# Optimization experiments

Measured on AMD Instinct MI355X. Metric: run time of the kernel, lower is better.

## Reference

```python
import jax, jax.numpy as jnp
import numpy as np

N, E, F_IN, H, MH, C, G = 100000, 3200000, 128, 32, 64, 10, 64

def _seg_sum(data, ids, num):
    return jax.ops.segment_sum(data, ids, num_segments=num)

def gcn_conv(x, row, col, ew, W, b, n):
    # PyG GCNConv: linear first, then self-loops + symmetric edge-weight norm + scatter-add
    h = x @ W  # [N, H]
    loop = jnp.arange(n)
    r = jnp.concatenate([row, loop])
    c = jnp.concatenate([col, loop])
    w = jnp.concatenate([ew, jnp.ones((n,), dtype=ew.dtype)])
    deg = _seg_sum(w, c, n)
    dinv = jnp.where(deg > 0, jax.lax.rsqrt(deg), 0.0)
    norm = dinv[r] * w * dinv[c]  # [E+N]
    out = _seg_sum(norm[:, None] * h[r], c, n)  # scatter to targets
    return out + b

def setup_inputs():
    key = jax.random.key(0)
    ks = jax.random.split(key, 16)
    inp = {
        "x": jax.random.normal(ks[0], (N, F_IN), dtype=jnp.float32),
        "edge_index": jax.random.randint(ks[1], (2, E), 0, N, dtype=jnp.int64),
        "edge_weight": jax.random.uniform(ks[2], (E,), dtype=jnp.float32),
        "batch": jnp.sort(jax.random.randint(ks[3], (N,), 0, G, dtype=jnp.int64)),
    }
    def lin(k, i, o):
        s = 1.0 / np.sqrt(i)
        k1, k2 = jax.random.split(k)
        return (jax.random.uniform(k1, (i, o), minval=-s, maxval=s, dtype=jnp.float32),
                jax.random.uniform(k2, (o,), minval=-s, maxval=s, dtype=jnp.float32))
    inp["W1"], inp["b1"] = lin(ks[4], F_IN, H)
    inp["W2"], inp["b2"] = lin(ks[5], H, H)
    inp["W3"], inp["b3"] = lin(ks[6], H, H)
    inp["Wm0"], inp["bm0"] = lin(ks[7], H, MH)
    inp["Wm1"], inp["bm1"] = lin(ks[8], MH, MH)
    inp["Wout"], inp["bout"] = lin(ks[9], MH, C)
    return inp

def reference(x, edge_index, edge_weight, batch, W1, b1, W2, b2, W3, b3, Wm0, bm0, Wm1, bm1, Wout, bout):
    row, col = edge_index[0], edge_index[1]
    h = jax.nn.relu(gcn_conv(x, row, col, edge_weight, W1, b1, N))
    h = jax.nn.relu(gcn_conv(h, row, col, edge_weight, W2, b2, N))
    h = gcn_conv(h, row, col, edge_weight, W3, b3, N)
    # global mean pool over graphs
    sums = _seg_sum(h, batch, G)
    counts = _seg_sum(jnp.ones((N,), dtype=h.dtype), batch, G)
    g = sums / jnp.maximum(counts, 1.0)[:, None]
    # dropout p=0.5 is identity at inference (training=False)
    g = jax.nn.relu(g @ Wm0 + bm0)
    g = jax.nn.relu(g @ Wm1 + bm1)
    return g @ Wout + bout
```

## Files before the change

### kernel.cpp

```cpp
#include <hip/hip_runtime.h>

#define NN 100000
#define NE 3200000
#define FIN 128
#define HID 32
#define MH  64
#define NC  10
#define NG  64
#define NBKT 782
#define NBLK 512
#define EPB  (NE / NBLK)
#define SCANL (NBKT * NBLK)
#define SRCMASK 0x1FFFF
#define BCAP 5120

typedef float floatx2 __attribute__((ext_vector_type(2)));

__global__ __launch_bounds__(1024)
void hist_bkt(const int* __restrict__ ei, int* __restrict__ cnt2) {
    __shared__ int h[NBKT];
    int tid = threadIdx.x, blk = blockIdx.x;
    for (int b = tid; b < NBKT; b += 1024) h[b] = 0;
    __syncthreads();
    int base = blk * EPB;
    for (int i = tid; i < EPB; i += 1024)
        atomicAdd(&h[ei[NE + base + i] >> 7], 1);
    __syncthreads();
    for (int b = tid; b < NBKT; b += 1024) cnt2[b * NBLK + blk] = h[b];
}

__global__ void scan_block(const int* __restrict__ in, int* __restrict__ out,
                           int* __restrict__ bsum, int n) {
    __shared__ int lds[256];
    int tid = threadIdx.x;
    int base = blockIdx.x * 1024 + tid * 4;
    int v0 = 0, v1 = 0, v2 = 0, v3 = 0;
    if (base + 0 < n) v0 = in[base + 0];
    if (base + 1 < n) v1 = in[base + 1];
    if (base + 2 < n) v2 = in[base + 2];
    if (base + 3 < n) v3 = in[base + 3];
    int s = v0 + v1 + v2 + v3;
    lds[tid] = s;
    __syncthreads();
    for (int off = 1; off < 256; off <<= 1) {
        int val = (tid >= off) ? lds[tid - off] : 0;
        __syncthreads();
        lds[tid] += val;
        __syncthreads();
    }
    int excl = lds[tid] - s;
    if (tid == 255) bsum[blockIdx.x] = lds[255];
    if (base + 0 < n) out[base + 0] = excl;
    if (base + 1 < n) out[base + 1] = excl + v0;
    if (base + 2 < n) out[base + 2] = excl + v0 + v1;
    if (base + 3 < n) out[base + 3] = excl + v0 + v1 + v2;
}

__global__ void scan_top(int* __restrict__ bsum, int nb, float* __restrict__ sc) {
    int lane = threadIdx.x;
    for (int i = lane; i < NG * HID + NG; i += 64) sc[i] = 0.0f;
    int carry = 0;
    for (int base = 0; base < nb; base += 64) {
        int i = base + lane;
        int orig = (i < nb) ? bsum[i] : 0;
        int v = orig;
#pragma unroll
        for (int off = 1; off < 64; off <<= 1) {
            int t = __shfl_up(v, off, 64);
            if (lane >= off) v += t;
        }
        if (i < nb) bsum[i] = carry + v - orig;
        carry += __shfl(v, 63, 64);
    }
}

__global__ void scan_add(int* __restrict__ data, const int* __restrict__ bsum, int n) {
    int i = blockIdx.x * 256 + threadIdx.x;
    if (i < n) data[i] += bsum[i >> 10];
}

__global__ __launch_bounds__(1024)
void scatter_bkt(const int* __restrict__ ei, const float* __restrict__ ew,
                 const int* __restrict__ cnt2, const int* __restrict__ scanned,
                 int2* __restrict__ tre) {
    __shared__ int2 pay[EPB];
    __shared__ int scur[NBKT];
    __shared__ int hexc[NBKT];
    __shared__ int gbase[NBKT];
    int tid = threadIdx.x, blk = blockIdx.x;
    int myh = 0;
    if (tid < NBKT) {
        myh = cnt2[tid * NBLK + blk];
        gbase[tid] = scanned[tid * NBLK + blk];
        scur[tid] = myh;
    }
    __syncthreads();
    for (int off = 1; off < NBKT; off <<= 1) {
        int v = (tid < NBKT && tid >= off) ? scur[tid - off] : 0;
        __syncthreads();
        if (tid < NBKT) scur[tid] += v;
        __syncthreads();
    }
    if (tid < NBKT) { int ex = scur[tid] - myh; hexc[tid] = ex; scur[tid] = ex; }
    __syncthreads();
    int base = blk * EPB;
    for (int i = tid; i < EPB; i += 1024) {
        int e = base + i;
        int c = ei[NE + e];
        int r = ei[e];
        unsigned int wb = __float_as_uint(ew[e]);
        int b = c >> 7;
        int j = atomicAdd(&scur[b], 1);
        pay[j] = make_int2(r | ((c & 127) << 17) | ((b & 0xFF) << 24),
                           (int)((wb & ~3u) | ((unsigned)b >> 8)));
    }
    __syncthreads();
    for (int j = tid; j < EPB; j += 1024) {
        int2 q = pay[j];
        int b = (int)((((unsigned)q.y & 3u) << 8) | (((unsigned)q.x >> 24) & 0xFFu));
        int pos = gbase[b] + (j - hexc[b]);
        tre[pos] = make_int2(q.x & 0x00FFFFFF, q.y & ~3);
    }
}

__global__ __launch_bounds__(512)
void sort_k(const int2* __restrict__ tre, const int* __restrict__ scanned,
            unsigned int* __restrict__ srn4, int* __restrict__ rowptr,
            float* __restrict__ dinv) {
    __shared__ int2 ed[BCAP];
    __shared__ int h[128];
    __shared__ float dw[128];
    __shared__ int cur[128];
    int b = blockIdx.x, tid = threadIdx.x;
    int base = scanned[b * NBLK];
    int end = (b == NBKT - 1) ? NE : scanned[(b + 1) * NBLK];
    int n = end - base;
    bool staged = (n <= BCAP);
    if (tid < 128) { h[tid] = 0; dw[tid] = 0.f; }
    __syncthreads();
    for (int i = tid; i < n; i += 512) {
        int2 q = tre[base + i];
        if (staged) ed[i] = q;
        int key = (q.x >> 17) & 127;
        atomicAdd(&h[key], 1);
        atomicAdd(&dw[key], __int_as_float(q.y));
    }
    __syncthreads();
    if (tid < 64) {
        int lane = tid;
        int carry = 0;
#pragma unroll
        for (int c = 0; c < 2; ++c) {
            int idx = c * 64 + lane;
            int hv = h[idx];
            int v = hv;
#pragma unroll
            for (int off = 1; off < 64; off <<= 1) {
                int t = __shfl_up(v, off, 64);
                if (lane >= off) v += t;
            }
            cur[idx] = base + carry + v - hv;
            int node = b * 128 + idx;
            if (node < NN) {
                rowptr[node] = base + carry + v;
                dinv[node] = rsqrtf(1.0f + dw[idx]);
            }
            carry += __shfl(v, 63, 64);
        }
    }
    __syncthreads();
    for (int i = tid; i < n; i += 512) {
        int2 q = staged ? ed[i] : tre[base + i];
        int key = (q.x >> 17) & 127;
        int pos = atomicAdd(&cur[key], 1);
        unsigned int wb = (unsigned)q.y;
        wb += 0x7FFFu + ((wb >> 16) & 1u);
        srn4[pos] = (unsigned)(q.x & SRCMASK) | (((wb >> 16) & 0x7FFFu) << 17);
    }
}

template <int IN_DIM, bool RELU_IN>
__global__ __launch_bounds__(256)
void linear_k(const float* __restrict__ in, const float* __restrict__ W,
              const float* __restrict__ dinv, unsigned int* __restrict__ tmp8) {
    constexpr int J4 = IN_DIM / 4;
    constexpr int XSS = J4 + 1;
    __shared__ float4 xs[64 * XSS];
    __shared__ float4 wp[IN_DIM * 8];
    int tid = threadIdx.x;
    for (int idx = tid; idx < IN_DIM * 8; idx += 256) {
        int j = idx >> 3, kg = idx & 7;
        const float* wr = W + j * 32 + kg * 4;
        wp[idx] = make_float4(wr[0], wr[1], wr[2], wr[3]);
    }
    int rbase = blockIdx.x * 64;
    const float4* in4 = (const float4*)in;
    for (int idx = tid; idx < 64 * J4; idx += 256) {
        int row = idx / J4, j4 = idx % J4;
        int grow = rbase + row;
        float4 v = (grow < NN) ? in4[(size_t)grow * J4 + j4]
                               : make_float4(0.f, 0.f, 0.f, 0.f);
        if (RELU_IN) {
            v.x = fmaxf(v.x, 0.f); v.y = fmaxf(v.y, 0.f);
            v.z = fmaxf(v.z, 0.f); v.w = fmaxf(v.w, 0.f);
        }
        xs[row * XSS + j4] = v;
    }
    __syncthreads();
    int kg = tid & 7;
    int rp = tid >> 3;
    int r0 = rbase + 2 * rp;
    if (r0 >= NN) return;
    const float4* x0 = &xs[(2 * rp) * XSS];
    const float4* x1 = &xs[(2 * rp + 1) * XSS];
    float a00 = 0, a01 = 0, a02 = 0, a03 = 0;
    float a10 = 0, a11 = 0, a12 = 0, a13 = 0;
#pragma unroll
    for (int j4 = 0; j4 < J4; ++j4) {
        float4 v0 = x0[j4], v1 = x1[j4];
        const float4* wj = &wp[j4 * 4 * 8 + kg];
        float4 w0 = wj[0], w1 = wj[8], w2 = wj[16], w3 = wj[24];
#define LSTEP(VX0, VX1, W4) \
        a00 = fmaf(VX0, W4.x, a00); a01 = fmaf(VX0, W4.y, a01); \
        a02 = fmaf(VX0, W4.z, a02); a03 = fmaf(VX0, W4.w, a03); \
        a10 = fmaf(VX1, W4.x, a10); a11 = fmaf(VX1, W4.y, a11); \
        a12 = fmaf(VX1, W4.z, a12); a13 = fmaf(VX1, W4.w, a13);
        LSTEP(v0.x, v1.x, w0)
        LSTEP(v0.y, v1.y, w1)
        LSTEP(v0.z, v1.z, w2)
        LSTEP(v0.w, v1.w, w3)
#undef LSTEP
    }
    float d0 = dinv[r0], d1 = dinv[r0 + 1];
    a00 *= d0; a01 *= d0; a02 *= d0; a03 *= d0;
    a10 *= d1; a11 *= d1; a12 *= d1; a13 *= d1;
    int q0 = __builtin_amdgcn_cvt_pk_fp8_f32(a00, a01, 0, false);
    q0 = __builtin_amdgcn_cvt_pk_fp8_f32(a02, a03, q0, true);
    int q1 = __builtin_amdgcn_cvt_pk_fp8_f32(a10, a11, 0, false);
    q1 = __builtin_amdgcn_cvt_pk_fp8_f32(a12, a13, q1, true);
    tmp8[r0 * 8 + kg] = (unsigned int)q0;
    tmp8[(r0 + 1) * 8 + kg] = (unsigned int)q1;
}

__global__ void aggregate(const unsigned int* __restrict__ srn4,
                          const int* __restrict__ rowptr,
                          const float* __restrict__ dinv,
                          const float* __restrict__ bias,
                          const unsigned int* __restrict__ tmp8,
                          float* __restrict__ h) {
    int wid = (blockIdx.x * 256 + threadIdx.x) >> 6;
    if (wid >= NN) return;
    int lane = threadIdx.x & 63;
    int g = lane >> 3;
    int q = lane & 7;
    int end = rowptr[wid];
    int start = (wid == 0) ? 0 : rowptr[wid - 1];
    float a0 = 0, a1 = 0, a2 = 0, a3 = 0;
    float b0 = 0, b1 = 0, b2 = 0, b3 = 0;
    int e = start + g;
    for (; e + 24 < end; e += 32) {
        unsigned int p0 = srn4[e];
        unsigned int p1 = srn4[e + 8];
        unsigned int p2 = srn4[e + 16];
        unsigned int p3 = srn4[e + 24];
        unsigned int u0 = tmp8[(size_t)(p0 & SRCMASK) * 8 + q];
        unsigned int u1 = tmp8[(size_t)(p1 & SRCMASK) * 8 + q];
        unsigned int u2 = tmp8[(size_t)(p2 & SRCMASK) * 8 + q];
        unsigned int u3 = tmp8[(size_t)(p3 & SRCMASK) * 8 + q];
        float w0 = __uint_as_float((p0 >> 1) & 0x7FFF0000u);
        float w1 = __uint_as_float((p1 >> 1) & 0x7FFF0000u);
        float w2 = __uint_as_float((p2 >> 1) & 0x7FFF0000u);
        float w3 = __uint_as_float((p3 >> 1) & 0x7FFF0000u);
        floatx2 lo, hi;
        lo = __builtin_amdgcn_cvt_pk_f32_fp8(u0, false);
        hi = __builtin_amdgcn_cvt_pk_f32_fp8(u0, true);
        a0 = fmaf(w0, lo.x, a0); a1 = fmaf(w0, lo.y, a1);
        a2 = fmaf(w0, hi.x, a2); a3 = fmaf(w0, hi.y, a3);
        lo = __builtin_amdgcn_cvt_pk_f32_fp8(u1, false);
        hi = __builtin_amdgcn_cvt_pk_f32_fp8(u1, true);
        b0 = fmaf(w1, lo.x, b0); b1 = fmaf(w1, lo.y, b1);
        b2 = fmaf(w1, hi.x, b2); b3 = fmaf(w1, hi.y, b3);
        lo = __builtin_amdgcn_cvt_pk_f32_fp8(u2, false);
        hi = __builtin_amdgcn_cvt_pk_f32_fp8(u2, true);
        a0 = fmaf(w2, lo.x, a0); a1 = fmaf(w2, lo.y, a1);
        a2 = fmaf(w2, hi.x, a2); a3 = fmaf(w2, hi.y, a3);
        lo = __builtin_amdgcn_cvt_pk_f32_fp8(u3, false);
        hi = __builtin_amdgcn_cvt_pk_f32_fp8(u3, true);
        b0 = fmaf(w3, lo.x, b0); b1 = fmaf(w3, lo.y, b1);
        b2 = fmaf(w3, hi.x, b2); b3 = fmaf(w3, hi.y, b3);
    }
    for (; e < end; e += 8) {
        unsigned int p = srn4[e];
        unsigned int u = tmp8[(size_t)(p & SRCMASK) * 8 + q];
        float w = __uint_as_float((p >> 1) & 0x7FFF0000u);
        floatx2 lo = __builtin_amdgcn_cvt_pk_f32_fp8(u, false);
        floatx2 hi = __builtin_amdgcn_cvt_pk_f32_fp8(u, true);
        a0 = fmaf(w, lo.x, a0); a1 = fmaf(w, lo.y, a1);
        a2 = fmaf(w, hi.x, a2); a3 = fmaf(w, hi.y, a3);
    }
    a0 += b0; a1 += b1; a2 += b2; a3 += b3;
    a0 += __shfl_xor(a0, 8, 64); a1 += __shfl_xor(a1, 8, 64);
    a2 += __shfl_xor(a2, 8, 64); a3 += __shfl_xor(a3, 8, 64);
    a0 += __shfl_xor(a0, 16, 64); a1 += __shfl_xor(a1, 16, 64);
    a2 += __shfl_xor(a2, 16, 64); a3 += __shfl_xor(a3, 16, 64);
    a0 += __shfl_xor(a0, 32, 64); a1 += __shfl_xor(a1, 32, 64);
    a2 += __shfl_xor(a2, 32, 64); a3 += __shfl_xor(a3, 32, 64);
    if (g == 0) {
        float d = dinv[wid];
        unsigned int sv = tmp8[(size_t)wid * 8 + q];
        floatx2 slo = __builtin_amdgcn_cvt_pk_f32_fp8(sv, false);
        floatx2 shi = __builtin_amdgcn_cvt_pk_f32_fp8(sv, true);
        float4 bq = ((const float4*)bias)[q];
        float4 o;
        o.x = bq.x + d * (slo.x + a0);
        o.y = bq.y + d * (slo.y + a1);
        o.z = bq.z + d * (shi.x + a2);
        o.w = bq.w + d * (shi.y + a3);
        ((float4*)(h + (size_t)wid * HID))[q] = o;
    }
}

__global__ void pool_k(const float* __restrict__ h, const int* __restrict__ batch,
                       float* __restrict__ sums, float* __restrict__ counts) {
    int t = blockIdx.x * 256 + threadIdx.x;
    int chunk = t >> 5, k = t & 31;
    int n0 = chunk * 32;
    if (n0 >= NN) return;
    int n1 = min(n0 + 32, NN);
    int g = batch[n0];
    float acc = 0.f, cacc = 0.f;
    for (int i = n0; i < n1; ++i) {
        int gi = batch[i];
        if (gi != g) {
            atomicAdd(&sums[g * HID + k], acc);
            if (k == 0) atomicAdd(&counts[g], cacc);
            g = gi; acc = 0.f; cacc = 0.f;
        }
        acc += h[(size_t)i * HID + k];
        cacc += 1.f;
    }
    atomicAdd(&sums[g * HID + k], acc);
    if (k == 0) atomicAdd(&counts[g], cacc);
}

__global__ __launch_bounds__(64)
void mlp_k(const float* __restrict__ sums, const float* __restrict__ counts,
           const float* __restrict__ Wm0, const float* __restrict__ bm0,
           const float* __restrict__ Wm1, const float* __restrict__ bm1,
           const float* __restrict__ Wout, const float* __restrict__ bout,
           float* __restrict__ out) {
    __shared__ float g0[HID];
    __shared__ float g1[MH];
    __shared__ float g2[MH];
    int g = blockIdx.x;
    int k = threadIdx.x;
    if (k < HID) g0[k] = sums[g * HID + k] / fmaxf(counts[g], 1.0f);
    __syncthreads();
    float acc = bm0[k];
#pragma unroll
    for (int j = 0; j < HID; ++j) acc = fmaf(g0[j], Wm0[j * MH + k], acc);
    g1[k] = fmaxf(acc, 0.f);
    __syncthreads();
    float acc2 = bm1[k];
#pragma unroll
    for (int j = 0; j < MH; ++j) acc2 = fmaf(g1[j], Wm1[j * MH + k], acc2);
    g2[k] = fmaxf(acc2, 0.f);
    __syncthreads();
    if (k < NC) {
        float acc3 = bout[k];
#pragma unroll
        for (int j = 0; j < MH; ++j) acc3 = fmaf(g2[j], Wout[j * NC + k], acc3);
        out[g * NC + k] = acc3;
    }
}

extern "C" void kernel_launch(void* const* d_in, const int* in_sizes, int n_in,
                              void* d_out, int out_size, void* d_ws, size_t ws_size,
                              hipStream_t stream) {
    const float* x    = (const float*)d_in[0];
    const int*   ei   = (const int*)d_in[1];
    const float* ew   = (const float*)d_in[2];
    const int*   batch= (const int*)d_in[3];
    const float* W1   = (const float*)d_in[4];
    const float* b1   = (const float*)d_in[5];
    const float* W2   = (const float*)d_in[6];
    const float* b2   = (const float*)d_in[7];
    const float* W3   = (const float*)d_in[8];
    const float* b3   = (const float*)d_in[9];
    const float* Wm0  = (const float*)d_in[10];
    const float* bm0  = (const float*)d_in[11];
    const float* Wm1  = (const float*)d_in[12];
    const float* bm1  = (const float*)d_in[13];
    const float* Wout = (const float*)d_in[14];
    const float* bout = (const float*)d_in[15];
    float* out = (float*)d_out;

    char* p = (char*)d_ws;
    unsigned int* srn4 = (unsigned int*)p; p += sizeof(unsigned int) * (size_t)NE;
    char*  S   = p;                      p += 12 * (size_t)NE;
    int2*  tre = (int2*)S;
    int*   cnt2    = (int*)(S + sizeof(int2) * (size_t)NE);
    int*   scanned = cnt2 + SCANL;
    unsigned int* tmp8 = (unsigned int*)S;
    float* hA  = (float*)(S + (size_t)NN * HID);
    float* hB  = hA + (size_t)NN * HID;
    int*   bsum    = (int*)p;            p += sizeof(int) * 512;
    float* dinv    = (float*)p;          p += sizeof(float) * NN;
    int*   rowptr  = (int*)p;            p += sizeof(int) * NN;
    float* sums    = (float*)p;          p += sizeof(float) * NG * HID;
    float* counts  = (float*)p;

    dim3 blk(256);
    const int NB_SCAN = (SCANL + 1023) / 1024;
    const int NB_LIN = (NN + 63) / 64;

    hist_bkt<<<NBLK, 1024, 0, stream>>>(ei, cnt2);
    scan_block<<<NB_SCAN, blk, 0, stream>>>(cnt2, scanned, bsum, SCANL);
    scan_top<<<1, 64, 0, stream>>>(bsum, NB_SCAN, sums);
    scan_add<<<(SCANL + 255) / 256, blk, 0, stream>>>(scanned, bsum, SCANL);
    scatter_bkt<<<NBLK, 1024, 0, stream>>>(ei, ew, cnt2, scanned, tre);
    sort_k<<<NBKT, 512, 0, stream>>>(tre, scanned, srn4, rowptr, dinv);

    linear_k<FIN, false><<<NB_LIN, blk, 0, stream>>>(x, W1, dinv, tmp8);
    aggregate<<<25000, blk, 0, stream>>>(srn4, rowptr, dinv, b1, tmp8, hA);
    linear_k<HID, true><<<NB_LIN, blk, 0, stream>>>(hA, W2, dinv, tmp8);
    aggregate<<<25000, blk, 0, stream>>>(srn4, rowptr, dinv, b2, tmp8, hB);
    linear_k<HID, true><<<NB_LIN, blk, 0, stream>>>(hB, W3, dinv, tmp8);
    aggregate<<<25000, blk, 0, stream>>>(srn4, rowptr, dinv, b3, tmp8, hA);

    pool_k<<<391, blk, 0, stream>>>(hA, batch, sums, counts);
    mlp_k<<<NG, 64, 0, stream>>>(sums, counts, Wm0, bm0, Wm1, bm1, Wout, bout, out);
}
```

Measured before the change: 405.8 us.

## Fuse GCN aggregation with next layer's linear transform and FP8 quantization

A new agg_lin kernel runs the neighbor aggregation for each node, applies bias and ReLU, and then multiplies the row by the next layer's weight matrix. The row goes through per-wave shared memory, and the kernel writes dinv-scaled FP8 features for the next layer directly. It replaces the first two aggregate plus linear_k pairs, removing two kernel launches and the FP32 hidden-state write and re-read between them. In exchange, the aggregation kernel does extra per-node work and reuses shared memory within a wave with no explicit barrier. It also needs ping-pong FP8 buffers.

```diff
diff --git a/kernel.cpp b/kernel.cpp
--- a/kernel.cpp
+++ b/kernel.cpp
@@ -242,6 +242,63 @@
     tmp8[(r0 + 1) * 8 + kg] = (unsigned int)q1;
 }
 
+#define AGG_BODY \
+    int lane = threadIdx.x & 63; \
+    int g = lane >> 3; \
+    int q = lane & 7; \
+    int end = rowptr[wid]; \
+    int start = (wid == 0) ? 0 : rowptr[wid - 1]; \
+    float a0 = 0, a1 = 0, a2 = 0, a3 = 0; \
+    float b0 = 0, b1 = 0, b2 = 0, b3 = 0; \
+    int e = start + g; \
+    for (; e + 24 < end; e += 32) { \
+        unsigned int p0 = srn4[e]; \
+        unsigned int p1 = srn4[e + 8]; \
+        unsigned int p2 = srn4[e + 16]; \
+        unsigned int p3 = srn4[e + 24]; \
+        unsigned int u0 = tmp8[(size_t)(p0 & SRCMASK) * 8 + q]; \
+        unsigned int u1 = tmp8[(size_t)(p1 & SRCMASK) * 8 + q]; \
+        unsigned int u2 = tmp8[(size_t)(p2 & SRCMASK) * 8 + q]; \
+        unsigned int u3 = tmp8[(size_t)(p3 & SRCMASK) * 8 + q]; \
+        float w0 = __uint_as_float((p0 >> 1) & 0x7FFF0000u); \
+        float w1 = __uint_as_float((p1 >> 1) & 0x7FFF0000u); \
+        float w2 = __uint_as_float((p2 >> 1) & 0x7FFF0000u); \
+        float w3 = __uint_as_float((p3 >> 1) & 0x7FFF0000u); \
+        floatx2 lo, hi; \
+        lo = __builtin_amdgcn_cvt_pk_f32_fp8(u0, false); \
+        hi = __builtin_amdgcn_cvt_pk_f32_fp8(u0, true); \
+        a0 = fmaf(w0, lo.x, a0); a1 = fmaf(w0, lo.y, a1); \
+        a2 = fmaf(w0, hi.x, a2); a3 = fmaf(w0, hi.y, a3); \
+        lo = __builtin_amdgcn_cvt_pk_f32_fp8(u1, false); \
+        hi = __builtin_amdgcn_cvt_pk_f32_fp8(u1, true); \
+        b0 = fmaf(w1, lo.x, b0); b1 = fmaf(w1, lo.y, b1); \
+        b2 = fmaf(w1, hi.x, b2); b3 = fmaf(w1, hi.y, b3); \
+        lo = __builtin_amdgcn_cvt_pk_f32_fp8(u2, false); \
+        hi = __builtin_amdgcn_cvt_pk_f32_fp8(u2, true); \
+        a0 = fmaf(w2, lo.x, a0); a1 = fmaf(w2, lo.y, a1); \
+        a2 = fmaf(w2, hi.x, a2); a3 = fmaf(w2, hi.y, a3); \
+        lo = __builtin_amdgcn_cvt_pk_f32_fp8(u3, false); \
+        hi = __builtin_amdgcn_cvt_pk_f32_fp8(u3, true); \
+        b0 = fmaf(w3, lo.x, b0); b1 = fmaf(w3, lo.y, b1); \
+        b2 = fmaf(w3, hi.x, b2); b3 = fmaf(w3, hi.y, b3); \
+    } \
+    for (; e < end; e += 8) { \
+        unsigned int p = srn4[e]; \
+        unsigned int u = tmp8[(size_t)(p & SRCMASK) * 8 + q]; \
+        float w = __uint_as_float((p >> 1) & 0x7FFF0000u); \
+        floatx2 lo = __builtin_amdgcn_cvt_pk_f32_fp8(u, false); \
+        floatx2 hi = __builtin_amdgcn_cvt_pk_f32_fp8(u, true); \
+        a0 = fmaf(w, lo.x, a0); a1 = fmaf(w, lo.y, a1); \
+        a2 = fmaf(w, hi.x, a2); a3 = fmaf(w, hi.y, a3); \
+    } \
+    a0 += b0; a1 += b1; a2 += b2; a3 += b3; \
+    a0 += __shfl_xor(a0, 8, 64); a1 += __shfl_xor(a1, 8, 64); \
+    a2 += __shfl_xor(a2, 8, 64); a3 += __shfl_xor(a3, 8, 64); \
+    a0 += __shfl_xor(a0, 16, 64); a1 += __shfl_xor(a1, 16, 64); \
+    a2 += __shfl_xor(a2, 16, 64); a3 += __shfl_xor(a3, 16, 64); \
+    a0 += __shfl_xor(a0, 32, 64); a1 += __shfl_xor(a1, 32, 64); \
+    a2 += __shfl_xor(a2, 32, 64); a3 += __shfl_xor(a3, 32, 64);
+
 __global__ void aggregate(const unsigned int* __restrict__ srn4,
                           const int* __restrict__ rowptr,
                           const float* __restrict__ dinv,
@@ -250,61 +307,7 @@
                           float* __restrict__ h) {
     int wid = (blockIdx.x * 256 + threadIdx.x) >> 6;
     if (wid >= NN) return;
-    int lane = threadIdx.x & 63;
-    int g = lane >> 3;
-    int q = lane & 7;
-    int end = rowptr[wid];
-    int start = (wid == 0) ? 0 : rowptr[wid - 1];
-    float a0 = 0, a1 = 0, a2 = 0, a3 = 0;
-    float b0 = 0, b1 = 0, b2 = 0, b3 = 0;
-    int e = start + g;
-    for (; e + 24 < end; e += 32) {
-        unsigned int p0 = srn4[e];
-        unsigned int p1 = srn4[e + 8];
-        unsigned int p2 = srn4[e + 16];
-        unsigned int p3 = srn4[e + 24];
-        unsigned int u0 = tmp8[(size_t)(p0 & SRCMASK) * 8 + q];
-        unsigned int u1 = tmp8[(size_t)(p1 & SRCMASK) * 8 + q];
-        unsigned int u2 = tmp8[(size_t)(p2 & SRCMASK) * 8 + q];
-        unsigned int u3 = tmp8[(size_t)(p3 & SRCMASK) * 8 + q];
-        float w0 = __uint_as_float((p0 >> 1) & 0x7FFF0000u);
-        float w1 = __uint_as_float((p1 >> 1) & 0x7FFF0000u);
-        float w2 = __uint_as_float((p2 >> 1) & 0x7FFF0000u);
-        float w3 = __uint_as_float((p3 >> 1) & 0x7FFF0000u);
-        floatx2 lo, hi;
-        lo = __builtin_amdgcn_cvt_pk_f32_fp8(u0, false);
-        hi = __builtin_amdgcn_cvt_pk_f32_fp8(u0, true);
-        a0 = fmaf(w0, lo.x, a0); a1 = fmaf(w0, lo.y, a1);
-        a2 = fmaf(w0, hi.x, a2); a3 = fmaf(w0, hi.y, a3);
-        lo = __builtin_amdgcn_cvt_pk_f32_fp8(u1, false);
-        hi = __builtin_amdgcn_cvt_pk_f32_fp8(u1, true);
-        b0 = fmaf(w1, lo.x, b0); b1 = fmaf(w1, lo.y, b1);
-        b2 = fmaf(w1, hi.x, b2); b3 = fmaf(w1, hi.y, b3);
-        lo = __builtin_amdgcn_cvt_pk_f32_fp8(u2, false);
-        hi = __builtin_amdgcn_cvt_pk_f32_fp8(u2, true);
-        a0 = fmaf(w2, lo.x, a0); a1 = fmaf(w2, lo.y, a1);
-        a2 = fmaf(w2, hi.x, a2); a3 = fmaf(w2, hi.y, a3);
-        lo = __builtin_amdgcn_cvt_pk_f32_fp8(u3, false);
-        hi = __builtin_amdgcn_cvt_pk_f32_fp8(u3, true);
-        b0 = fmaf(w3, lo.x, b0); b1 = fmaf(w3, lo.y, b1);
-        b2 = fmaf(w3, hi.x, b2); b3 = fmaf(w3, hi.y, b3);
-    }
-    for (; e < end; e += 8) {
-        unsigned int p = srn4[e];
-        unsigned int u = tmp8[(size_t)(p & SRCMASK) * 8 + q];
-        float w = __uint_as_float((p >> 1) & 0x7FFF0000u);
-        floatx2 lo = __builtin_amdgcn_cvt_pk_f32_fp8(u, false);
-        floatx2 hi = __builtin_amdgcn_cvt_pk_f32_fp8(u, true);
-        a0 = fmaf(w, lo.x, a0); a1 = fmaf(w, lo.y, a1);
-        a2 = fmaf(w, hi.x, a2); a3 = fmaf(w, hi.y, a3);
-    }
-    a0 += b0; a1 += b1; a2 += b2; a3 += b3;
-    a0 += __shfl_xor(a0, 8, 64); a1 += __shfl_xor(a1, 8, 64);
-    a2 += __shfl_xor(a2, 8, 64); a3 += __shfl_xor(a3, 8, 64);
-    a0 += __shfl_xor(a0, 16, 64); a1 += __shfl_xor(a1, 16, 64);
-    a2 += __shfl_xor(a2, 16, 64); a3 += __shfl_xor(a3, 16, 64);
-    a0 += __shfl_xor(a0, 32, 64); a1 += __shfl_xor(a1, 32, 64);
-    a2 += __shfl_xor(a2, 32, 64); a3 += __shfl_xor(a3, 32, 64);
+    AGG_BODY
     if (g == 0) {
         float d = dinv[wid];
         unsigned int sv = tmp8[(size_t)wid * 8 + q];
@@ -317,6 +320,52 @@
         o.z = bq.z + d * (shi.x + a2);
         o.w = bq.w + d * (shi.y + a3);
         ((float4*)(h + (size_t)wid * HID))[q] = o;
+    }
+}
+
+__global__ void agg_lin(const unsigned int* __restrict__ srn4,
+                        const int* __restrict__ rowptr,
+                        const float* __restrict__ dinv,
+                        const float* __restrict__ bias,
+                        const float* __restrict__ Wn,
+                        const unsigned int* __restrict__ tmp8,
+                        unsigned int* __restrict__ tmp8_out) {
+    __shared__ float hrow[4][HID];
+    int wid = (blockIdx.x * 256 + threadIdx.x) >> 6;
+    if (wid >= NN) return;
+    int wv = threadIdx.x >> 6;
+    AGG_BODY
+    float d = dinv[wid];
+    if (g == 0) {
+        unsigned int sv = tmp8[(size_t)wid * 8 + q];
+        floatx2 slo = __builtin_amdgcn_cvt_pk_f32_fp8(sv, false);
+        floatx2 shi = __builtin_amdgcn_cvt_pk_f32_fp8(sv, true);
+        float4 bq = ((const float4*)bias)[q];
+        float4 o;
+        o.x = fmaxf(bq.x + d * (slo.x + a0), 0.f);
+        o.y = fmaxf(bq.y + d * (slo.y + a1), 0.f);
+        o.z = fmaxf(bq.z + d * (shi.x + a2), 0.f);
+        o.w = fmaxf(bq.w + d * (shi.y + a3), 0.f);
+        *((float4*)&hrow[wv][4 * q]) = o;
+    }
+    int j = lane & 31, half = lane >> 5;
+    const float* hr = hrow[wv];
+    const float* wc = Wn + j;
+    float y = 0.f;
+#pragma unroll
+    for (int k = 0; k < 16; ++k) {
+        int kk = half * 16 + k;
+        y = fmaf(hr[kk], wc[kk * 32], y);
+    }
+    y += __shfl_xor(y, 32, 64);
+    y *= d;
+    float y1 = __shfl_down(y, 1, 64);
+    float y2 = __shfl_down(y, 2, 64);
+    float y3 = __shfl_down(y, 3, 64);
+    if (half == 0 && (j & 3) == 0) {
+        int w0 = __builtin_amdgcn_cvt_pk_fp8_f32(y, y1, 0, false);
+        w0 = __builtin_amdgcn_cvt_pk_fp8_f32(y2, y3, w0, true);
+        tmp8_out[wid * 8 + (j >> 2)] = (unsigned int)w0;
     }
 }
 
@@ -401,9 +450,9 @@
     int2*  tre = (int2*)S;
     int*   cnt2    = (int*)(S + sizeof(int2) * (size_t)NE);
     int*   scanned = cnt2 + SCANL;
-    unsigned int* tmp8 = (unsigned int*)S;
-    float* hA  = (float*)(S + (size_t)NN * HID);
-    float* hB  = hA + (size_t)NN * HID;
+    unsigned int* tmp8  = (unsigned int*)S;
+    unsigned int* tmp8b = tmp8 + (size_t)NN * 8;
+    float* hA  = (float*)(S + 2 * (size_t)NN * HID);
     int*   bsum    = (int*)p;            p += sizeof(int) * 512;
     float* dinv    = (float*)p;          p += sizeof(float) * NN;
     int*   rowptr  = (int*)p;            p += sizeof(int) * NN;
@@ -422,10 +471,8 @@
     sort_k<<<NBKT, 512, 0, stream>>>(tre, scanned, srn4, rowptr, dinv);
 
     linear_k<FIN, false><<<NB_LIN, blk, 0, stream>>>(x, W1, dinv, tmp8);
-    aggregate<<<25000, blk, 0, stream>>>(srn4, rowptr, dinv, b1, tmp8, hA);
-    linear_k<HID, true><<<NB_LIN, blk, 0, stream>>>(hA, W2, dinv, tmp8);
-    aggregate<<<25000, blk, 0, stream>>>(srn4, rowptr, dinv, b2, tmp8, hB);
-    linear_k<HID, true><<<NB_LIN, blk, 0, stream>>>(hB, W3, dinv, tmp8);
+    agg_lin<<<25000, blk, 0, stream>>>(srn4, rowptr, dinv, b1, W2, tmp8, tmp8b);
+    agg_lin<<<25000, blk, 0, stream>>>(srn4, rowptr, dinv, b2, W3, tmp8b, tmp8);
     aggregate<<<25000, blk, 0, stream>>>(srn4, rowptr, dinv, b3, tmp8, hA);
 
     pool_k<<<391, blk, 0, stream>>>(hA, batch, sums, counts);
```

Result: no change. 404.2 us (median of 2 runs) (-0.4%).
